# Performance work log

Hardware: AMD Instinct MI355X
Metric: run time of the kernel (lower is better)

## Reference

```python
import jax, jax.numpy as jnp
import numpy as np

N_NODES = 100000
N_EDGES = 1600000
IN_DIM, HID_DIM, OUT_DIM = 128, 128, 64
BN_EPS = 1e-5


def _norm_edges(edge_index, n):
    # PyG GCNConv: add self-loops, symmetric normalization deg^-1/2
    loop = jnp.arange(n, dtype=edge_index.dtype)
    src = jnp.concatenate([edge_index[0], loop])
    dst = jnp.concatenate([edge_index[1], loop])
    deg = jax.ops.segment_sum(jnp.ones_like(dst, dtype=jnp.float32), dst, num_segments=n)
    dinv = jnp.where(deg > 0, jax.lax.rsqrt(deg), 0.0)
    norm = dinv[src] * dinv[dst]  # [E+N]
    return src, dst, norm


def _gcn_conv(x, src, dst, norm, W, b):
    h = x @ W                      # [N, d_out]
    msg = h[src] * norm[:, None]   # [E+N, d_out] gather + scale
    out = jax.ops.segment_sum(msg, dst, num_segments=x.shape[0])  # scatter-add
    return out + b


def _bn(x, g, be):
    mu = x.mean(axis=0)
    var = x.var(axis=0)
    return (x - mu) * jax.lax.rsqrt(var + BN_EPS) * g + be


def setup_inputs() -> dict:
    key = jax.random.key(0)
    ks = jax.random.split(key, 6)
    s1 = (1.0 / np.sqrt(IN_DIM)).astype(np.float32)
    s2 = (1.0 / np.sqrt(HID_DIM)).astype(np.float32)
    return {
        "x": jax.random.normal(ks[0], (N_NODES, IN_DIM), dtype=jnp.float32),
        "edge_index": jax.random.randint(ks[1], (2, N_EDGES), 0, N_NODES, dtype=jnp.int32),
        "W1": jax.random.normal(ks[2], (IN_DIM, HID_DIM), dtype=jnp.float32) * s1,
        "b1": jnp.zeros((HID_DIM,), jnp.float32),
        "g1": jnp.ones((HID_DIM,), jnp.float32),
        "be1": jnp.zeros((HID_DIM,), jnp.float32),
        "W2": jax.random.normal(ks[3], (HID_DIM, HID_DIM), dtype=jnp.float32) * s2,
        "b2": jnp.zeros((HID_DIM,), jnp.float32),
        "g2": jnp.ones((HID_DIM,), jnp.float32),
        "be2": jnp.zeros((HID_DIM,), jnp.float32),
        "W3": jax.random.normal(ks[4], (HID_DIM, OUT_DIM), dtype=jnp.float32) * s2,
        "b3": jnp.zeros((OUT_DIM,), jnp.float32),
    }


def reference(x, edge_index, W1, b1, g1, be1, W2, b2, g2, be2, W3, b3):
    src, dst, norm = _norm_edges(edge_index, x.shape[0])
    h = jax.nn.relu(_bn(_gcn_conv(x, src, dst, norm, W1, b1), g1, be1))
    h = jax.nn.relu(_bn(_gcn_conv(h, src, dst, norm, W2, b2), g2, be2))
    return _gcn_conv(h, src, dst, norm, W3, b3)
```

## Files before the change

kernel.cpp:

```cpp
#include <hip/hip_runtime.h>

#define N_NODES 100000
#define N_EDGES 1600000
#define PAD 48
#define NB 391
#define NBLK 256
#define EPB (N_EDGES / NBLK)
#define SCAN_N (NB * NBLK)

using bf16x8 = __attribute__((ext_vector_type(8))) short;
using f32x4  = __attribute__((ext_vector_type(4))) float;


__device__ __forceinline__ float bflo(unsigned u) { return __uint_as_float(u << 16); }
__device__ __forceinline__ float bfhi(unsigned u) { return __uint_as_float(u & 0xffff0000u); }
__device__ __forceinline__ unsigned packbf(float a, float b) {
    unsigned ua = __float_as_uint(a), ub = __float_as_uint(b);
    ua = ua + 0x7fffu + ((ua >> 16) & 1u);
    ub = ub + 0x7fffu + ((ub >> 16) & 1u);
    return (ua >> 16) | (ub & 0xffff0000u);
}


__global__ __launch_bounds__(256) void hist_kernel(const int* __restrict__ dst,
                                                   int* __restrict__ counts) {
    __shared__ int hist[NB];
    int tid = threadIdx.x, blk = blockIdx.x;
    for (int i = tid; i < NB; i += 256) hist[i] = 0;
    __syncthreads();
    int s0 = blk * EPB;
    for (int k = tid; k < EPB; k += 256)
        atomicAdd(&hist[dst[s0 + k] >> 8], 1);
    __syncthreads();
    for (int b = tid; b < NB; b += 256) counts[b * NBLK + blk] = hist[b];
}

__global__ __launch_bounds__(1024) void scan1_kernel(const int* __restrict__ cnt,
                                                     int* __restrict__ off,
                                                     int* __restrict__ bsum, int n) {
    __shared__ int wsum[17];
    int tid = threadIdx.x, lane = tid & 63, w = tid >> 6;
    int i = blockIdx.x * 1024 + tid;
    int v = (i < n) ? cnt[i] : 0;
    int x = v;
    #pragma unroll
    for (int d = 1; d < 64; d <<= 1) {
        int y = __shfl_up(x, d, 64);
        if (lane >= d) x += y;
    }
    if (lane == 63) wsum[w] = x;
    __syncthreads();
    if (tid == 0) {
        int s = 0;
        #pragma unroll
        for (int j = 0; j < 16; j++) { int t = wsum[j]; wsum[j] = s; s += t; }
        wsum[16] = s;
    }
    __syncthreads();
    if (i < n) off[i + 1] = x + wsum[w];
    if (tid == 0) bsum[blockIdx.x] = wsum[16];
}

__global__ void scan2_kernel(int* __restrict__ bsum, int nb, float* __restrict__ stats1,
                             float* __restrict__ stats2) {
    int t = threadIdx.x;
    stats1[t] = 0.f;
    stats2[t] = 0.f;
    if (t == 0) {
        int s = 0;
        for (int j = 0; j < nb; j++) { int v = bsum[j]; bsum[j] = s; s += v; }
    }
}

__device__ __forceinline__ int off_at(const int* __restrict__ off_raw,
                                      const int* __restrict__ bsum, int idx) {
    return idx ? off_raw[idx] + bsum[(idx - 1) >> 10] : 0;
}

__global__ __launch_bounds__(256) void part_kernel(const int* __restrict__ src,
                                                   const int* __restrict__ dst,
                                                   const int* __restrict__ off_raw,
                                                   const int* __restrict__ bsum,
                                                   unsigned* __restrict__ ebuf) {
    __shared__ int cur[NB];
    int tid = threadIdx.x, blk = blockIdx.x;
    for (int b = tid; b < NB; b += 256)
        cur[b] = off_at(off_raw, bsum, b * NBLK + blk);
    __syncthreads();
    int s0 = blk * EPB;
    for (int k = tid; k < EPB; k += 256) {
        int s = src[s0 + k], d = dst[s0 + k];
        int pos = atomicAdd(&cur[d >> 8], 1);
        ebuf[pos] = (unsigned)s | ((unsigned)(d & 255) << 17);
    }
}

__global__ __launch_bounds__(256) void bucket_kernel(const unsigned* __restrict__ ebuf,
                                                     const int* __restrict__ off_raw,
                                                     const int* __restrict__ bsum,
                                                     int* __restrict__ esrc_pad,
                                                     int* __restrict__ cnt,
                                                     float* __restrict__ dinv, int n) {
    __shared__ int epad[256 * PAD];
    __shared__ int cur[256];
    int tid = threadIdx.x, b = blockIdx.x;
    int start = off_at(off_raw, bsum, b * NBLK);
    int end = off_at(off_raw, bsum, (b + 1) * NBLK);
    cur[tid] = 0;
    __syncthreads();
    for (int e = start + tid; e < end; e += 256) {
        unsigned sd = ebuf[e];
        int ld = sd >> 17;
        int pos = atomicAdd(&cur[ld], 1);
        if (pos < PAD) epad[ld * PAD + pos] = (int)(sd & 0x1FFFFu);
    }
    __syncthreads();
    int nd0 = b << 8;
    int nn = min(256, n - nd0);
    if (tid < nn) {
        cnt[nd0 + tid] = cur[tid];
        dinv[nd0 + tid] = rsqrtf((float)(cur[tid] + 1));
    }
    int tot = nn * PAD;
    for (int i = tid; i < tot; i += 256) esrc_pad[(size_t)nd0 * PAD + i] = epad[i];
}


__global__ void wconv3_kernel(const float* __restrict__ W1, const float* __restrict__ W2,
                              const float* __restrict__ W3, unsigned* __restrict__ Wt1,
                              unsigned* __restrict__ Wt2, unsigned* __restrict__ Wt3) {
    int b = blockIdx.x;
    const float* W;
    unsigned* Wt;
    int M, i;
    if (b < 32)      { W = W1; Wt = Wt1; M = 128; i = b * 256 + threadIdx.x; }
    else if (b < 64) { W = W2; Wt = Wt2; M = 128; i = (b - 32) * 256 + threadIdx.x; }
    else             { W = W3; Wt = Wt3; M = 64;  i = (b - 64) * 256 + threadIdx.x; }
    if (i >= M * 64) return;
    int m = i >> 6, ku = i & 63;
    Wt[(size_t)m * 64 + ku] = packbf(W[(size_t)(2 * ku) * M + m], W[(size_t)(2 * ku + 1) * M + m]);
}


template <int M, int MODE>
__global__ __launch_bounds__(256) void gemm_mfma_kernel(const void* __restrict__ Xv,
                                                        const unsigned* __restrict__ Wt,
                                                        const float* __restrict__ stats,
                                                        const float* __restrict__ g,
                                                        const float* __restrict__ be,
                                                        unsigned* __restrict__ H, int n) {
    __shared__ float sls[256];
    if constexpr (MODE == 1) {
        int t = threadIdx.x;
        if (t < 128) {
            float inv_n = 1.f / (float)n;
            float mu = stats[t] * inv_n;
            float var = stats[128 + t] * inv_n - mu * mu;
            float sc = g[t] * rsqrtf(var + 1e-5f);
            sls[t] = sc;
            sls[128 + t] = be[t] - mu * sc;
        }
        __syncthreads();
    }
    int wid = threadIdx.x >> 6, lane = threadIdx.x & 63;
    int r0 = (blockIdx.x * 4 + wid) * 16;
    if (r0 >= n) return;
    int rl = lane & 15, kg = lane >> 4;
    int row = r0 + rl;

    bf16x8 xf[4];
    if constexpr (MODE == 0) {
        const float* X = (const float*)Xv;
        #pragma unroll
        for (int ks = 0; ks < 4; ks++) {
            const float* p = &X[(size_t)row * 128 + ks * 32 + kg * 8];
            float4 f0 = *(const float4*)p;
            float4 f1 = *(const float4*)(p + 4);
            unsigned o[4] = { packbf(f0.x, f0.y), packbf(f0.z, f0.w),
                              packbf(f1.x, f1.y), packbf(f1.z, f1.w) };
            xf[ks] = *(bf16x8*)o;
        }
    } else {
        const unsigned* X = (const unsigned*)Xv;
        #pragma unroll
        for (int ks = 0; ks < 4; ks++) {
            int c = ks * 32 + kg * 8;
            uint4 u = *(const uint4*)&X[(size_t)row * 64 + (c >> 1)];
            float4 sc0 = *(const float4*)&sls[c];
            float4 sc1 = *(const float4*)&sls[c + 4];
            float4 sh0 = *(const float4*)&sls[128 + c];
            float4 sh1 = *(const float4*)&sls[128 + c + 4];
            float v0 = fmaxf(bflo(u.x) * sc0.x + sh0.x, 0.f);
            float v1 = fmaxf(bfhi(u.x) * sc0.y + sh0.y, 0.f);
            float v2 = fmaxf(bflo(u.y) * sc0.z + sh0.z, 0.f);
            float v3 = fmaxf(bfhi(u.y) * sc0.w + sh0.w, 0.f);
            float v4 = fmaxf(bflo(u.z) * sc1.x + sh1.x, 0.f);
            float v5 = fmaxf(bfhi(u.z) * sc1.y + sh1.y, 0.f);
            float v6 = fmaxf(bflo(u.w) * sc1.z + sh1.z, 0.f);
            float v7 = fmaxf(bfhi(u.w) * sc1.w + sh1.w, 0.f);
            unsigned o[4] = { packbf(v0, v1), packbf(v2, v3), packbf(v4, v5), packbf(v6, v7) };
            xf[ks] = *(bf16x8*)o;
        }
    }

    constexpr int NCB = M / 16;
    f32x4 acc[NCB];
    #pragma unroll
    for (int cb = 0; cb < NCB; cb++) acc[cb] = (f32x4){0.f, 0.f, 0.f, 0.f};

    #pragma unroll
    for (int cb = 0; cb < NCB; cb++) {
        #pragma unroll
        for (int ks = 0; ks < 4; ks++) {
            bf16x8 wf = *(const bf16x8*)&Wt[(size_t)(cb * 16 + rl) * 64 + ks * 16 + kg * 4];
            acc[cb] = __builtin_amdgcn_mfma_f32_16x16x32_bf16(wf, xf[ks], acc[cb], 0, 0, 0);
        }
    }

    unsigned* Hrow = &H[(size_t)row * (M / 2)];
    #pragma unroll
    for (int cb = 0; cb < NCB; cb++) {
        uint2 o;
        o.x = packbf(acc[cb][0], acc[cb][1]);
        o.y = packbf(acc[cb][2], acc[cb][3]);
        *(uint2*)&Hrow[cb * 8 + kg * 2] = o;
    }
}


__global__ __launch_bounds__(256) void agg128_kernel(const unsigned* __restrict__ H,
                                                     const int* __restrict__ cnt,
                                                     const int* __restrict__ esrc_pad,
                                                     const float* __restrict__ dinv,
                                                     const float* __restrict__ bias,
                                                     unsigned* __restrict__ out, int n) {
    int node = (blockIdx.x * blockDim.x + threadIdx.x) >> 6;
    int lane = threadIdx.x & 63;
    if (node >= n) return;
    float dn = dinv[node];
    float2 b = *(const float2*)&bias[lane * 2];
    int c = min(cnt[node], PAD);
    int s_l = (lane < c) ? esrc_pad[(size_t)node * PAD + lane] : node;
    float w_l = (lane < c) ? dinv[s_l] * dn : 0.f;
    unsigned u0 = H[(size_t)node * 64 + lane];
    float acc0 = dn * dn * bflo(u0), acc1 = dn * dn * bfhi(u0);
    for (int j = 0; j < c; j += 16) {
        unsigned u[16];
        int sr[16];
        float wr[16];
        #pragma unroll
        for (int t = 0; t < 16; t++) {
            sr[t] = __builtin_amdgcn_readlane(s_l, j + t);
            wr[t] = __uint_as_float(__builtin_amdgcn_readlane(__float_as_uint(w_l), j + t));
            u[t] = H[(size_t)sr[t] * 64 + lane];
        }
        #pragma unroll
        for (int t = 0; t < 16; t++) {
            acc0 += wr[t] * bflo(u[t]);
            acc1 += wr[t] * bfhi(u[t]);
        }
    }
    out[(size_t)node * 64 + lane] = packbf(acc0 + b.x, acc1 + b.y);
}

__global__ __launch_bounds__(256) void agg64_kernel(const unsigned short* __restrict__ H,
                                                    const int* __restrict__ cnt,
                                                    const int* __restrict__ esrc_pad,
                                                    const float* __restrict__ dinv,
                                                    const float* __restrict__ bias,
                                                    float* __restrict__ out, int n) {
    int node = (blockIdx.x * blockDim.x + threadIdx.x) >> 6;
    int lane = threadIdx.x & 63;
    if (node >= n) return;
    float dn = dinv[node];
    float bb = bias[lane];
    int c = min(cnt[node], PAD);
    int s_l = (lane < c) ? esrc_pad[(size_t)node * PAD + lane] : node;
    float w_l = (lane < c) ? dinv[s_l] * dn : 0.f;
    float acc = dn * dn * __uint_as_float(((unsigned)H[(size_t)node * 64 + lane]) << 16);
    for (int j = 0; j < c; j += 16) {
        unsigned short u[16];
        int sr[16];
        float wr[16];
        #pragma unroll
        for (int t = 0; t < 16; t++) {
            sr[t] = __builtin_amdgcn_readlane(s_l, j + t);
            wr[t] = __uint_as_float(__builtin_amdgcn_readlane(__float_as_uint(w_l), j + t));
            u[t] = H[(size_t)sr[t] * 64 + lane];
        }
        #pragma unroll
        for (int t = 0; t < 16; t++) {
            acc += wr[t] * __uint_as_float(((unsigned)u[t]) << 16);
        }
    }
    out[(size_t)node * 64 + lane] = acc + bb;
}


__global__ __launch_bounds__(256) void bnstats_kernel(const unsigned* __restrict__ X,
                                                      float* __restrict__ stats, int n) {
    int tid = threadIdx.x;
    int cpair = (tid & 31) * 2;
    int c0 = cpair * 2;
    int rg = tid >> 5;
    float s0 = 0, s1 = 0, s2 = 0, s3 = 0, q0 = 0, q1 = 0, q2 = 0, q3 = 0;
    int r0 = blockIdx.x * 512;
    int rend = min(r0 + 512, n);
    for (int r = r0 + rg; r < rend; r += 8) {
        uint2 u = *(const uint2*)&X[(size_t)r * 64 + cpair];
        float f0 = bflo(u.x), f1 = bfhi(u.x), f2 = bflo(u.y), f3 = bfhi(u.y);
        s0 += f0; q0 += f0 * f0;
        s1 += f1; q1 += f1 * f1;
        s2 += f2; q2 += f2 * f2;
        s3 += f3; q3 += f3 * f3;
    }
    __shared__ float ls[8][128], lq[8][128];
    ls[rg][c0] = s0; ls[rg][c0 + 1] = s1; ls[rg][c0 + 2] = s2; ls[rg][c0 + 3] = s3;
    lq[rg][c0] = q0; lq[rg][c0 + 1] = q1; lq[rg][c0 + 2] = q2; lq[rg][c0 + 3] = q3;
    __syncthreads();
    if (tid < 128) {
        float s = 0, q = 0;
        #pragma unroll
        for (int j = 0; j < 8; j++) { s += ls[j][tid]; q += lq[j][tid]; }
        atomicAdd(&stats[tid], s);
        atomicAdd(&stats[128 + tid], q);
    }
}


extern "C" void kernel_launch(void* const* d_in, const int* in_sizes, int n_in,
                              void* d_out, int out_size, void* d_ws, size_t ws_size,
                              hipStream_t stream) {
    const float* x  = (const float*)d_in[0];
    const int*   ei = (const int*)d_in[1];
    const float* W1 = (const float*)d_in[2];
    const float* b1 = (const float*)d_in[3];
    const float* g1 = (const float*)d_in[4];
    const float* be1 = (const float*)d_in[5];
    const float* W2 = (const float*)d_in[6];
    const float* b2 = (const float*)d_in[7];
    const float* g2 = (const float*)d_in[8];
    const float* be2 = (const float*)d_in[9];
    const float* W3 = (const float*)d_in[10];
    const float* b3 = (const float*)d_in[11];
    float* out = (float*)d_out;

    const int n = N_NODES, E = N_EDGES;
    const int* src = ei;
    const int* dst = ei + E;
    const int gemmGrid = (n + 63) / 64;
    const int nbScan = (SCAN_N + 1023) / 1024;

    char* p = (char*)d_ws;
    auto alloc = [&](size_t bytes) {
        void* r = (void*)p;
        p += (bytes + 255) & ~(size_t)255;
        return r;
    };
    int*      counts   = (int*)alloc((size_t)SCAN_N * 4);
    int*      off      = (int*)alloc((size_t)(SCAN_N + 1) * 4);
    int*      bsum     = (int*)alloc((size_t)nbScan * 4);
    unsigned* ebuf     = (unsigned*)alloc((size_t)E * 4);
    int*      cnt      = (int*)alloc((size_t)n * 4);
    float*    dinv     = (float*)alloc((size_t)n * 4);
    int*      esrc_pad = (int*)alloc((size_t)n * PAD * 4);
    unsigned* Hb       = (unsigned*)alloc((size_t)n * 64 * 4);
    unsigned* Ab       = (unsigned*)alloc((size_t)n * 64 * 4);
    unsigned* Wt1      = (unsigned*)alloc(128 * 64 * 4);
    unsigned* Wt2      = (unsigned*)alloc(128 * 64 * 4);
    unsigned* Wt3      = (unsigned*)alloc(64 * 64 * 4);
    float*    stats1   = (float*)alloc(256 * 4);
    float*    stats2   = (float*)alloc(256 * 4);

    hist_kernel<<<NBLK, 256, 0, stream>>>(dst, counts);
    scan1_kernel<<<nbScan, 1024, 0, stream>>>(counts, off, bsum, SCAN_N);
    scan2_kernel<<<1, 256, 0, stream>>>(bsum, nbScan, stats1, stats2);
    part_kernel<<<NBLK, 256, 0, stream>>>(src, dst, off, bsum, ebuf);
    bucket_kernel<<<NB, 256, 0, stream>>>(ebuf, off, bsum, esrc_pad, cnt, dinv, n);

    wconv3_kernel<<<80, 256, 0, stream>>>(W1, W2, W3, Wt1, Wt2, Wt3);

    gemm_mfma_kernel<128, 0><<<gemmGrid, 256, 0, stream>>>(x, Wt1, nullptr, nullptr, nullptr, Hb, n);
    agg128_kernel<<<n / 4, 256, 0, stream>>>(Hb, cnt, esrc_pad, dinv, b1, Ab, n);
    bnstats_kernel<<<(n + 511) / 512, 256, 0, stream>>>(Ab, stats1, n);

    gemm_mfma_kernel<128, 1><<<gemmGrid, 256, 0, stream>>>(Ab, Wt2, stats1, g1, be1, Hb, n);
    agg128_kernel<<<n / 4, 256, 0, stream>>>(Hb, cnt, esrc_pad, dinv, b2, Ab, n);
    bnstats_kernel<<<(n + 511) / 512, 256, 0, stream>>>(Ab, stats2, n);

    gemm_mfma_kernel<64, 1><<<gemmGrid, 256, 0, stream>>>(Ab, Wt3, stats2, g2, be2, Hb, n);
    agg64_kernel<<<n / 4, 256, 0, stream>>>((const unsigned short*)Hb, cnt, esrc_pad, dinv, b3, out, n);
}
```

Before: 364.8 us.

## Fuse BN stats into aggregation and merge preprocessing kernels into fewer launches

Folds the BatchNorm sum and sum-of-squares reduction into the aggregation kernel. Partial results go to 64 partitioned slots to reduce atomic contention, and the next GEMM reduces them. The weight conversion and stats zeroing are merged into the histogram launch, and the first-layer GEMM is co-scheduled with edge partitioning in one grid. The block-sum scan is parallelised. This removes separate passes over the activations and several launches, in exchange for extra atomics and heavier combined kernels.

```diff
diff --git a/kernel.cpp b/kernel.cpp
--- a/kernel.cpp
+++ b/kernel.cpp
@@ -7,6 +7,7 @@
 #define NBLK 256
 #define EPB (N_EDGES / NBLK)
 #define SCAN_N (NB * NBLK)
+#define NPART 64
 
 using bf16x8 = __attribute__((ext_vector_type(8))) short;
 using f32x4  = __attribute__((ext_vector_type(4))) float;
@@ -22,18 +23,46 @@
 }
 
 
-__global__ __launch_bounds__(256) void hist_kernel(const int* __restrict__ dst,
-                                                   int* __restrict__ counts) {
+__global__ __launch_bounds__(256) void histW_kernel(const int* __restrict__ dst,
+                                                    int* __restrict__ counts,
+                                                    const float* __restrict__ W1,
+                                                    const float* __restrict__ W2,
+                                                    const float* __restrict__ W3,
+                                                    unsigned* __restrict__ Wt1,
+                                                    unsigned* __restrict__ Wt2,
+                                                    unsigned* __restrict__ Wt3,
+                                                    float* __restrict__ stats1,
+                                                    float* __restrict__ stats2) {
     __shared__ int hist[NB];
-    int tid = threadIdx.x, blk = blockIdx.x;
-    for (int i = tid; i < NB; i += 256) hist[i] = 0;
-    __syncthreads();
-    int s0 = blk * EPB;
-    for (int k = tid; k < EPB; k += 256)
-        atomicAdd(&hist[dst[s0 + k] >> 8], 1);
-    __syncthreads();
-    for (int b = tid; b < NB; b += 256) counts[b * NBLK + blk] = hist[b];
-}
+    int tid = threadIdx.x, b = blockIdx.x;
+    if (b < 256) {
+        for (int i = tid; i < NB; i += 256) hist[i] = 0;
+        __syncthreads();
+        int s0 = b * EPB;
+        for (int k = tid; k < EPB; k += 256)
+            atomicAdd(&hist[dst[s0 + k] >> 8], 1);
+        __syncthreads();
+        for (int bb = tid; bb < NB; bb += 256) counts[bb * NBLK + b] = hist[bb];
+    } else if (b < 336) {
+        int wb = b - 256;
+        const float* W;
+        unsigned* Wt;
+        int M, i;
+        if (wb < 32)      { W = W1; Wt = Wt1; M = 128; i = wb * 256 + tid; }
+        else if (wb < 64) { W = W2; Wt = Wt2; M = 128; i = (wb - 32) * 256 + tid; }
+        else              { W = W3; Wt = Wt3; M = 64;  i = (wb - 64) * 256 + tid; }
+        if (i < M * 64) {
+            int m = i >> 6, ku = i & 63;
+            Wt[(size_t)m * 64 + ku] =
+                packbf(W[(size_t)(2 * ku) * M + m], W[(size_t)(2 * ku + 1) * M + m]);
+        }
+    } else {
+        int i = (b - 336) * 256 + tid;
+        stats1[i] = 0.f;
+        stats2[i] = 0.f;
+    }
+}
+
 
 __global__ __launch_bounds__(1024) void scan1_kernel(const int* __restrict__ cnt,
                                                      int* __restrict__ off,
@@ -61,15 +90,21 @@
     if (tid == 0) bsum[blockIdx.x] = wsum[16];
 }
 
-__global__ void scan2_kernel(int* __restrict__ bsum, int nb, float* __restrict__ stats1,
-                             float* __restrict__ stats2) {
+
+__global__ void scan2p_kernel(int* __restrict__ bsum, int nb) {
+    __shared__ int tmp[128];
     int t = threadIdx.x;
-    stats1[t] = 0.f;
-    stats2[t] = 0.f;
-    if (t == 0) {
-        int s = 0;
-        for (int j = 0; j < nb; j++) { int v = bsum[j]; bsum[j] = s; s += v; }
-    }
+    int v = (t < nb) ? bsum[t] : 0;
+    tmp[t] = v;
+    __syncthreads();
+    #pragma unroll
+    for (int d = 1; d < 128; d <<= 1) {
+        int u = (t >= d) ? tmp[t - d] : 0;
+        __syncthreads();
+        tmp[t] += u;
+        __syncthreads();
+    }
+    if (t < nb) bsum[t] = tmp[t] - v;
 }
 
 __device__ __forceinline__ int off_at(const int* __restrict__ off_raw,
@@ -77,23 +112,67 @@
     return idx ? off_raw[idx] + bsum[(idx - 1) >> 10] : 0;
 }
 
-__global__ __launch_bounds__(256) void part_kernel(const int* __restrict__ src,
-                                                   const int* __restrict__ dst,
-                                                   const int* __restrict__ off_raw,
-                                                   const int* __restrict__ bsum,
-                                                   unsigned* __restrict__ ebuf) {
+
+__global__ __launch_bounds__(256) void partG1_kernel(const int* __restrict__ src,
+                                                     const int* __restrict__ dst,
+                                                     const int* __restrict__ off_raw,
+                                                     const int* __restrict__ bsum,
+                                                     unsigned* __restrict__ ebuf,
+                                                     const float* __restrict__ X,
+                                                     const unsigned* __restrict__ Wt,
+                                                     unsigned* __restrict__ H, int n) {
     __shared__ int cur[NB];
-    int tid = threadIdx.x, blk = blockIdx.x;
-    for (int b = tid; b < NB; b += 256)
-        cur[b] = off_at(off_raw, bsum, b * NBLK + blk);
-    __syncthreads();
-    int s0 = blk * EPB;
-    for (int k = tid; k < EPB; k += 256) {
-        int s = src[s0 + k], d = dst[s0 + k];
-        int pos = atomicAdd(&cur[d >> 8], 1);
-        ebuf[pos] = (unsigned)s | ((unsigned)(d & 255) << 17);
-    }
-}
+    int tid = threadIdx.x;
+    if (blockIdx.x < NBLK) {
+        int blk = blockIdx.x;
+        for (int b = tid; b < NB; b += 256)
+            cur[b] = off_at(off_raw, bsum, b * NBLK + blk);
+        __syncthreads();
+        int s0 = blk * EPB;
+        for (int k = tid; k < EPB; k += 256) {
+            int s = src[s0 + k], d = dst[s0 + k];
+            int pos = atomicAdd(&cur[d >> 8], 1);
+            ebuf[pos] = (unsigned)s | ((unsigned)(d & 255) << 17);
+        }
+        return;
+    }
+    int gb = blockIdx.x - NBLK;
+    int wid = tid >> 6, lane = tid & 63;
+    int r0 = (gb * 4 + wid) * 16;
+    if (r0 >= n) return;
+    int rl = lane & 15, kg = lane >> 4;
+    int row = r0 + rl;
+    bf16x8 xf[4];
+    #pragma unroll
+    for (int ks = 0; ks < 4; ks++) {
+        const float* p = &X[(size_t)row * 128 + ks * 32 + kg * 8];
+        float4 f0 = *(const float4*)p;
+        float4 f1 = *(const float4*)(p + 4);
+        unsigned o[4] = { packbf(f0.x, f0.y), packbf(f0.z, f0.w),
+                          packbf(f1.x, f1.y), packbf(f1.z, f1.w) };
+        xf[ks] = *(bf16x8*)o;
+    }
+    f32x4 acc[8];
+    #pragma unroll
+    for (int cb = 0; cb < 8; cb++) acc[cb] = (f32x4){0.f, 0.f, 0.f, 0.f};
+    #pragma unroll
+    for (int cb = 0; cb < 8; cb++) {
+        #pragma unroll
+        for (int ks = 0; ks < 4; ks++) {
+            bf16x8 wf = *(const bf16x8*)&Wt[(size_t)(cb * 16 + rl) * 64 + ks * 16 + kg * 4];
+            acc[cb] = __builtin_amdgcn_mfma_f32_16x16x32_bf16(wf, xf[ks], acc[cb], 0, 0, 0);
+        }
+    }
+    unsigned* Hrow = &H[(size_t)row * 64];
+    #pragma unroll
+    for (int cb = 0; cb < 8; cb++) {
+        uint2 o;
+        o.x = packbf(acc[cb][0], acc[cb][1]);
+        o.y = packbf(acc[cb][2], acc[cb][3]);
+        *(uint2*)&Hrow[cb * 8 + kg * 2] = o;
+    }
+}
+
 
 __global__ __launch_bounds__(256) void bucket_kernel(const unsigned* __restrict__ ebuf,
                                                      const int* __restrict__ off_raw,
@@ -126,36 +205,26 @@
 }
 
 
-__global__ void wconv3_kernel(const float* __restrict__ W1, const float* __restrict__ W2,
-                              const float* __restrict__ W3, unsigned* __restrict__ Wt1,
-                              unsigned* __restrict__ Wt2, unsigned* __restrict__ Wt3) {
-    int b = blockIdx.x;
-    const float* W;
-    unsigned* Wt;
-    int M, i;
-    if (b < 32)      { W = W1; Wt = Wt1; M = 128; i = b * 256 + threadIdx.x; }
-    else if (b < 64) { W = W2; Wt = Wt2; M = 128; i = (b - 32) * 256 + threadIdx.x; }
-    else             { W = W3; Wt = Wt3; M = 64;  i = (b - 64) * 256 + threadIdx.x; }
-    if (i >= M * 64) return;
-    int m = i >> 6, ku = i & 63;
-    Wt[(size_t)m * 64 + ku] = packbf(W[(size_t)(2 * ku) * M + m], W[(size_t)(2 * ku + 1) * M + m]);
-}
-
-
-template <int M, int MODE>
-__global__ __launch_bounds__(256) void gemm_mfma_kernel(const void* __restrict__ Xv,
-                                                        const unsigned* __restrict__ Wt,
-                                                        const float* __restrict__ stats,
-                                                        const float* __restrict__ g,
-                                                        const float* __restrict__ be,
-                                                        unsigned* __restrict__ H, int n) {
+template <int M>
+__global__ __launch_bounds__(256) void gemmB_mfma_kernel(const unsigned* __restrict__ X,
+                                                         const unsigned* __restrict__ Wt,
+                                                         const float* __restrict__ stats,
+                                                         const float* __restrict__ g,
+                                                         const float* __restrict__ be,
+                                                         unsigned* __restrict__ H, int n) {
     __shared__ float sls[256];
-    if constexpr (MODE == 1) {
+    {
         int t = threadIdx.x;
         if (t < 128) {
+            float s = 0.f, q = 0.f;
+            #pragma unroll 8
+            for (int p2 = 0; p2 < NPART; p2++) {
+                s += stats[p2 * 256 + t];
+                q += stats[p2 * 256 + 128 + t];
+            }
             float inv_n = 1.f / (float)n;
-            float mu = stats[t] * inv_n;
-            float var = stats[128 + t] * inv_n - mu * mu;
+            float mu = s * inv_n;
+            float var = q * inv_n - mu * mu;
             float sc = g[t] * rsqrtf(var + 1e-5f);
             sls[t] = sc;
             sls[128 + t] = be[t] - mu * sc;
@@ -169,45 +238,30 @@
     int row = r0 + rl;
 
     bf16x8 xf[4];
-    if constexpr (MODE == 0) {
-        const float* X = (const float*)Xv;
-        #pragma unroll
-        for (int ks = 0; ks < 4; ks++) {
-            const float* p = &X[(size_t)row * 128 + ks * 32 + kg * 8];
-            float4 f0 = *(const float4*)p;
-            float4 f1 = *(const float4*)(p + 4);
-            unsigned o[4] = { packbf(f0.x, f0.y), packbf(f0.z, f0.w),
-                              packbf(f1.x, f1.y), packbf(f1.z, f1.w) };
-            xf[ks] = *(bf16x8*)o;
-        }
-    } else {
-        const unsigned* X = (const unsigned*)Xv;
-        #pragma unroll
-        for (int ks = 0; ks < 4; ks++) {
-            int c = ks * 32 + kg * 8;
-            uint4 u = *(const uint4*)&X[(size_t)row * 64 + (c >> 1)];
-            float4 sc0 = *(const float4*)&sls[c];
-            float4 sc1 = *(const float4*)&sls[c + 4];
-            float4 sh0 = *(const float4*)&sls[128 + c];
-            float4 sh1 = *(const float4*)&sls[128 + c + 4];
-            float v0 = fmaxf(bflo(u.x) * sc0.x + sh0.x, 0.f);
-            float v1 = fmaxf(bfhi(u.x) * sc0.y + sh0.y, 0.f);
-            float v2 = fmaxf(bflo(u.y) * sc0.z + sh0.z, 0.f);
-            float v3 = fmaxf(bfhi(u.y) * sc0.w + sh0.w, 0.f);
-            float v4 = fmaxf(bflo(u.z) * sc1.x + sh1.x, 0.f);
-            float v5 = fmaxf(bfhi(u.z) * sc1.y + sh1.y, 0.f);
-            float v6 = fmaxf(bflo(u.w) * sc1.z + sh1.z, 0.f);
-            float v7 = fmaxf(bfhi(u.w) * sc1.w + sh1.w, 0.f);
-            unsigned o[4] = { packbf(v0, v1), packbf(v2, v3), packbf(v4, v5), packbf(v6, v7) };
-            xf[ks] = *(bf16x8*)o;
-        }
+    #pragma unroll
+    for (int ks = 0; ks < 4; ks++) {
+        int c = ks * 32 + kg * 8;
+        uint4 u = *(const uint4*)&X[(size_t)row * 64 + (c >> 1)];
+        float4 sc0 = *(const float4*)&sls[c];
+        float4 sc1 = *(const float4*)&sls[c + 4];
+        float4 sh0 = *(const float4*)&sls[128 + c];
+        float4 sh1 = *(const float4*)&sls[128 + c + 4];
+        float v0 = fmaxf(bflo(u.x) * sc0.x + sh0.x, 0.f);
+        float v1 = fmaxf(bfhi(u.x) * sc0.y + sh0.y, 0.f);
+        float v2 = fmaxf(bflo(u.y) * sc0.z + sh0.z, 0.f);
+        float v3 = fmaxf(bfhi(u.y) * sc0.w + sh0.w, 0.f);
+        float v4 = fmaxf(bflo(u.z) * sc1.x + sh1.x, 0.f);
+        float v5 = fmaxf(bfhi(u.z) * sc1.y + sh1.y, 0.f);
+        float v6 = fmaxf(bflo(u.w) * sc1.z + sh1.z, 0.f);
+        float v7 = fmaxf(bfhi(u.w) * sc1.w + sh1.w, 0.f);
+        unsigned o[4] = { packbf(v0, v1), packbf(v2, v3), packbf(v4, v5), packbf(v6, v7) };
+        xf[ks] = *(bf16x8*)o;
     }
 
     constexpr int NCB = M / 16;
     f32x4 acc[NCB];
     #pragma unroll
     for (int cb = 0; cb < NCB; cb++) acc[cb] = (f32x4){0.f, 0.f, 0.f, 0.f};
-
     #pragma unroll
     for (int cb = 0; cb < NCB; cb++) {
         #pragma unroll
@@ -216,7 +270,6 @@
             acc[cb] = __builtin_amdgcn_mfma_f32_16x16x32_bf16(wf, xf[ks], acc[cb], 0, 0, 0);
         }
     }
-
     unsigned* Hrow = &H[(size_t)row * (M / 2)];
     #pragma unroll
     for (int cb = 0; cb < NCB; cb++) {
@@ -228,15 +281,16 @@
 }
 
 
-__global__ __launch_bounds__(256) void agg128_kernel(const unsigned* __restrict__ H,
-                                                     const int* __restrict__ cnt,
-                                                     const int* __restrict__ esrc_pad,
-                                                     const float* __restrict__ dinv,
-                                                     const float* __restrict__ bias,
-                                                     unsigned* __restrict__ out, int n) {
+__global__ __launch_bounds__(256) void agg128bn_kernel(const unsigned* __restrict__ H,
+                                                       const int* __restrict__ cnt,
+                                                       const int* __restrict__ esrc_pad,
+                                                       const float* __restrict__ dinv,
+                                                       const float* __restrict__ bias,
+                                                       unsigned* __restrict__ out,
+                                                       float* __restrict__ stats) {
     int node = (blockIdx.x * blockDim.x + threadIdx.x) >> 6;
     int lane = threadIdx.x & 63;
-    if (node >= n) return;
+    int wv = threadIdx.x >> 6;
     float dn = dinv[node];
     float2 b = *(const float2*)&bias[lane * 2];
     int c = min(cnt[node], PAD);
@@ -260,7 +314,22 @@
             acc1 += wr[t] * bfhi(u[t]);
         }
     }
-    out[(size_t)node * 64 + lane] = packbf(acc0 + b.x, acc1 + b.y);
+    float o0 = acc0 + b.x, o1 = acc1 + b.y;
+    out[(size_t)node * 64 + lane] = packbf(o0, o1);
+    __shared__ float ls[4][128], lq[4][128];
+    ls[wv][lane * 2] = o0;
+    ls[wv][lane * 2 + 1] = o1;
+    lq[wv][lane * 2] = o0 * o0;
+    lq[wv][lane * 2 + 1] = o1 * o1;
+    __syncthreads();
+    int t = threadIdx.x;
+    if (t < 128) {
+        float s = ls[0][t] + ls[1][t] + ls[2][t] + ls[3][t];
+        float q = lq[0][t] + lq[1][t] + lq[2][t] + lq[3][t];
+        float* sp = &stats[(blockIdx.x & (NPART - 1)) * 256];
+        atomicAdd(&sp[t], s);
+        atomicAdd(&sp[128 + t], q);
+    }
 }
 
 __global__ __launch_bounds__(256) void agg64_kernel(const unsigned short* __restrict__ H,
@@ -297,37 +366,6 @@
 }
 
 
-__global__ __launch_bounds__(256) void bnstats_kernel(const unsigned* __restrict__ X,
-                                                      float* __restrict__ stats, int n) {
-    int tid = threadIdx.x;
-    int cpair = (tid & 31) * 2;
-    int c0 = cpair * 2;
-    int rg = tid >> 5;
-    float s0 = 0, s1 = 0, s2 = 0, s3 = 0, q0 = 0, q1 = 0, q2 = 0, q3 = 0;
-    int r0 = blockIdx.x * 512;
-    int rend = min(r0 + 512, n);
-    for (int r = r0 + rg; r < rend; r += 8) {
-        uint2 u = *(const uint2*)&X[(size_t)r * 64 + cpair];
-        float f0 = bflo(u.x), f1 = bfhi(u.x), f2 = bflo(u.y), f3 = bfhi(u.y);
-        s0 += f0; q0 += f0 * f0;
-        s1 += f1; q1 += f1 * f1;
-        s2 += f2; q2 += f2 * f2;
-        s3 += f3; q3 += f3 * f3;
-    }
-    __shared__ float ls[8][128], lq[8][128];
-    ls[rg][c0] = s0; ls[rg][c0 + 1] = s1; ls[rg][c0 + 2] = s2; ls[rg][c0 + 3] = s3;
-    lq[rg][c0] = q0; lq[rg][c0 + 1] = q1; lq[rg][c0 + 2] = q2; lq[rg][c0 + 3] = q3;
-    __syncthreads();
-    if (tid < 128) {
-        float s = 0, q = 0;
-        #pragma unroll
-        for (int j = 0; j < 8; j++) { s += ls[j][tid]; q += lq[j][tid]; }
-        atomicAdd(&stats[tid], s);
-        atomicAdd(&stats[128 + tid], q);
-    }
-}
-
-
 extern "C" void kernel_launch(void* const* d_in, const int* in_sizes, int n_in,
                               void* d_out, int out_size, void* d_ws, size_t ws_size,
                               hipStream_t stream) {
@@ -369,25 +407,21 @@
     unsigned* Wt1      = (unsigned*)alloc(128 * 64 * 4);
     unsigned* Wt2      = (unsigned*)alloc(128 * 64 * 4);
     unsigned* Wt3      = (unsigned*)alloc(64 * 64 * 4);
-    float*    stats1   = (float*)alloc(256 * 4);
-    float*    stats2   = (float*)alloc(256 * 4);
-
-    hist_kernel<<<NBLK, 256, 0, stream>>>(dst, counts);
+    float*    stats1   = (float*)alloc((size_t)NPART * 256 * 4);
+    float*    stats2   = (float*)alloc((size_t)NPART * 256 * 4);
+
+    histW_kernel<<<400, 256, 0, stream>>>(dst, counts, W1, W2, W3, Wt1, Wt2, Wt3,
+                                          stats1, stats2);
     scan1_kernel<<<nbScan, 1024, 0, stream>>>(counts, off, bsum, SCAN_N);
-    scan2_kernel<<<1, 256, 0, stream>>>(bsum, nbScan, stats1, stats2);
-    part_kernel<<<NBLK, 256, 0, stream>>>(src, dst, off, bsum, ebuf);
+    scan2p_kernel<<<1, 128, 0, stream>>>(bsum, nbScan);
+    partG1_kernel<<<NBLK + gemmGrid, 256, 0, stream>>>(src, dst, off, bsum, ebuf,
+                                                       x, Wt1, Hb, n);
     bucket_kernel<<<NB, 256, 0, stream>>>(ebuf, off, bsum, esrc_pad, cnt, dinv, n);
 
-    wconv3_kernel<<<80, 256, 0, stream>>>(W1, W2, W3, Wt1, Wt2, Wt3);
-
-    gemm_mfma_kernel<128, 0><<<gemmGrid, 256, 0, stream>>>(x, Wt1, nullptr, nullptr, nullptr, Hb, n);
-    agg128_kernel<<<n / 4, 256, 0, stream>>>(Hb, cnt, esrc_pad, dinv, b1, Ab, n);
-    bnstats_kernel<<<(n + 511) / 512, 256, 0, stream>>>(Ab, stats1, n);
-
-    gemm_mfma_kernel<128, 1><<<gemmGrid, 256, 0, stream>>>(Ab, Wt2, stats1, g1, be1, Hb, n);
-    agg128_kernel<<<n / 4, 256, 0, stream>>>(Hb, cnt, esrc_pad, dinv, b2, Ab, n);
-    bnstats_kernel<<<(n + 511) / 512, 256, 0, stream>>>(Ab, stats2, n);
-
-    gemm_mfma_kernel<64, 1><<<gemmGrid, 256, 0, stream>>>(Ab, Wt3, stats2, g2, be2, Hb, n);
-    agg64_kernel<<<n / 4, 256, 0, stream>>>((const unsigned short*)Hb, cnt, esrc_pad, dinv, b3, out, n);
-}
+    agg128bn_kernel<<<n / 4, 256, 0, stream>>>(Hb, cnt, esrc_pad, dinv, b1, Ab, stats1);
+    gemmB_mfma_kernel<128><<<gemmGrid, 256, 0, stream>>>(Ab, Wt2, stats1, g1, be1, Hb, n);
+    agg128bn_kernel<<<n / 4, 256, 0, stream>>>(Hb, cnt, esrc_pad, dinv, b2, Ab, stats2);
+    gemmB_mfma_kernel<64><<<gemmGrid, 256, 0, stream>>>(Ab, Wt3, stats2, g2, be2, Hb, n);
+    agg64_kernel<<<n / 4, 256, 0, stream>>>((const unsigned short*)Hb, cnt, esrc_pad,
+                                            dinv, b3, out, n);
+}
```

Result: faster. 322.9 us, median of 2 (-11.5%).
